# Kernel optimization log

Hardware: AMD Instinct MI355X
Metric: run time of the kernel (lower is better)

## Reference

```python
import jax, jax.numpy as jnp
import numpy as np

B, K, S, L, D, A = 16, 128, 64, 2, 256, 500  # batch, beam, stack, layers, hidden, max_actions


def setup_inputs() -> dict:
    key = jax.random.key(0)
    k = jax.random.split(key, 8)
    return {
        "gen_ll": jax.random.normal(k[0], (B, K), jnp.float32),
        "trees": jax.random.normal(k[1], (B, K, S, D), jnp.float32),
        "hiddens": jax.random.normal(k[2], (B, K, S + 1, L, D), jnp.float32),
        "cells": jax.random.normal(k[3], (B, K, S + 1, L, D), jnp.float32),
        "actions": jax.random.randint(k[4], (B, K, A), 0, 100, dtype=jnp.int64)
        if jax.config.jax_enable_x64 else jax.random.randint(k[4], (B, K, A), 0, 100),
        "actions_pos": jax.random.randint(k[5], (B, K), 0, A - 1),
        "pointer": jax.random.randint(k[6], (B, K), 0, S),
        "beam_widths": jax.random.randint(k[7], (B,), 1, K + 1),  # >= 1 active beam per batch
    }


def _gather_beam(x, sort_idx):
    # gather along beam dim (axis=1) with broadcast over trailing dims
    idx = sort_idx.reshape(sort_idx.shape + (1,) * (x.ndim - 2))
    return jnp.take_along_axis(x, idx, axis=1)


def reference(gen_ll, trees, hiddens, cells, actions, actions_pos, pointer, beam_widths):
    # BeamItems.shrink(): mask beams outside active width, sort by score desc,
    # then reorder every parallel tensor (stack + action path) by sort_idx.
    order = jnp.arange(K)
    active = order[None, :] < beam_widths[:, None]                    # [B, K] active_idx_mask
    gen_ll_m = jnp.where(active, gen_ll, -jnp.inf)
    sort_idx = jnp.argsort(-gen_ll_m, axis=1)                          # descending sort
    gen_ll_s = jnp.take_along_axis(gen_ll_m, sort_idx, axis=1)

    trees_s = _gather_beam(trees, sort_idx)                            # stack.sort_by
    hiddens_s = _gather_beam(hiddens, sort_idx)
    cells_s = _gather_beam(cells, sort_idx)
    actions_s = _gather_beam(actions, sort_idx)                        # action_path.sort_by
    actions_pos_s = jnp.take_along_axis(actions_pos, sort_idx, axis=1)
    pointer_s = jnp.take_along_axis(pointer, sort_idx, axis=1)         # stack_state.sort_by

    new_beam_widths = jnp.minimum(beam_widths, K)
    # BeamItems.marginal_probs(): logsumexp over active beams (inactive already -inf)
    marginal = jax.nn.logsumexp(gen_ll_s, axis=1)                      # [B]
    # ActionPath.prev_actions(): gather at actions_pos
    prev_actions = jnp.take_along_axis(actions_s, actions_pos_s[:, :, None], axis=2)[:, :, 0]

    return (gen_ll_s, trees_s, hiddens_s, cells_s, marginal,
            actions_s, actions_pos_s, pointer_s, prev_actions, new_beam_widths)
```

## Files before the change

### kernel.cpp

```cpp
#include <hip/hip_runtime.h>
#include <math.h>

#define B 16
#define K 128
#define S 64
#define L 2
#define D 256
#define A 500

#define ROW4_TREES 4096
#define ROW4_HID   8320

#define NEG_BIG (-1.0e30f)

#define OFF_GENLL 0
#define OFF_TREES 2048
#define OFF_HID   33556480
#define OFF_CELLS 101713920
#define OFF_MARG  169871360
#define OFF_ACT   169871376
#define OFF_APOS  170895376
#define OFF_PTR   170897424
#define OFF_PREV  170899472
#define OFF_NBW   170901520

#define NB_SORT B
#define NB_ACT  (B * K)
#define NB_BIG  (3 * B * K)
#define GRID (NB_SORT + NB_ACT + NB_BIG)

template<int N4>
__device__ __forceinline__ void copy_row(const float4* __restrict__ s,
                                         float4* __restrict__ d, int tid)
{
    constexpr int FULL = N4 / 256;
    constexpr int REM  = N4 % 256;
#pragma unroll 8
    for (int i = 0; i < FULL; ++i)
        d[i * 256 + tid] = s[i * 256 + tid];
    if (REM && tid < REM)
        d[FULL * 256 + tid] = s[FULL * 256 + tid];
}

__global__ void __launch_bounds__(256)
k_fused(const float* __restrict__ gen_ll,
        const float4* __restrict__ trees,
        const float4* __restrict__ hiddens,
        const float4* __restrict__ cells,
        const int* __restrict__ actions,
        const int* __restrict__ actions_pos,
        const int* __restrict__ pointer,
        const int* __restrict__ beam_widths,
        float* __restrict__ out)
{
    __shared__ float key[K];
    __shared__ int   sidx[K];
    __shared__ float red[4];

    const int tid = threadIdx.x;
    const int bid = blockIdx.x;

    int type, b, k = 0, r = 0, seg = 0;
    if (bid < NB_SORT) {
        type = 0; b = bid;
    } else if (bid < NB_SORT + NB_ACT) {
        type = 1; r = bid - NB_SORT; b = r >> 7; k = r & 127;
    } else {
        type = 2;
        const int idx = bid - (NB_SORT + NB_ACT);
        seg = idx % 3; r = idx / 3; b = r >> 7; k = r & 127;
    }

    const int w = beam_widths[b];
    if (tid < K) key[tid] = (tid < w) ? gen_ll[b * K + tid] : NEG_BIG;
    __syncthreads();
    if (tid < K) {
        const float my = key[tid];
        int rank = 0;
#pragma unroll 16
        for (int i = 0; i < K; ++i) {
            const float ki = key[i];
            rank += (ki > my) || (ki == my && i < tid);
        }
        sidx[rank] = tid;
    }
    __syncthreads();

    if (type == 2) {
        const int j = sidx[k];
        if (seg == 0) {
            copy_row<ROW4_TREES>(trees + (size_t)(b * K + j) * ROW4_TREES,
                                 (float4*)(out + OFF_TREES) + (size_t)r * ROW4_TREES, tid);
        } else {
            const float4* src = (seg == 1) ? hiddens : cells;
            float* dst0 = out + ((seg == 1) ? OFF_HID : OFF_CELLS);
            copy_row<ROW4_HID>(src + (size_t)(b * K + j) * ROW4_HID,
                               (float4*)dst0 + (size_t)r * ROW4_HID, tid);
        }
    } else if (type == 1) {
        const int j = sidx[k];
        const int* s = actions + (size_t)(b * K + j) * A;
        float* d = out + OFF_ACT + (size_t)r * A;
        if (tid < A) d[tid] = (float)s[tid];
        const int t2 = tid + 256;
        if (t2 < A) d[t2] = (float)s[t2];
    } else {
        if (tid < K) {
            const int j = sidx[tid];
            out[OFF_GENLL + b * K + tid] = key[j];
            const int ap = actions_pos[b * K + j];
            out[OFF_APOS + b * K + tid] = (float)ap;
            out[OFF_PTR  + b * K + tid] = (float)pointer[b * K + j];
            out[OFF_PREV + b * K + tid] = (float)actions[(size_t)(b * K + j) * A + ap];
        }
        const float v = (tid < K) ? key[tid] : NEG_BIG;
        if (tid < 128) {
            float m = v;
#pragma unroll
            for (int mask = 32; mask >= 1; mask >>= 1)
                m = fmaxf(m, __shfl_xor(m, mask, 64));
            if ((tid & 63) == 0) red[tid >> 6] = m;
        }
        __syncthreads();
        const float m = fmaxf(red[0], red[1]);
        if (tid < 128) {
            float e = expf(v - m);
#pragma unroll
            for (int mask = 32; mask >= 1; mask >>= 1)
                e += __shfl_xor(e, mask, 64);
            if ((tid & 63) == 0) red[2 + (tid >> 6)] = e;
        }
        __syncthreads();
        if (tid == 0) {
            out[OFF_MARG + b] = m + logf(red[2] + red[3]);
            out[OFF_NBW + b] = (float)(w < K ? w : K);
        }
    }
}

extern "C" void kernel_launch(void* const* d_in, const int* in_sizes, int n_in,
                              void* d_out, int out_size, void* d_ws, size_t ws_size,
                              hipStream_t stream)
{
    const float* gen_ll      = (const float*)d_in[0];
    const float* trees       = (const float*)d_in[1];
    const float* hiddens     = (const float*)d_in[2];
    const float* cells       = (const float*)d_in[3];
    const int*   actions     = (const int*)d_in[4];
    const int*   actions_pos = (const int*)d_in[5];
    const int*   pointer     = (const int*)d_in[6];
    const int*   beam_widths = (const int*)d_in[7];
    float* out = (float*)d_out;

    k_fused<<<GRID, 256, 0, stream>>>(gen_ll, (const float4*)trees,
                                      (const float4*)hiddens, (const float4*)cells,
                                      actions, actions_pos, pointer, beam_widths, out);
}
```

Baseline: 282.6 us.

## Split hidden/cell rows into halves, use nontemporal batched copies, vectorize actions

Hidden and cell rows are split into two half-row work units so the block workload is balanced with the trees rows. The copy loop now issues eight nontemporal vector loads before eight nontemporal stores to raise memory-level parallelism and avoid cache pollution. The action gather is vectorized to int4 loads and float4 stores, blocks are reordered so big copies launch first, and launch bounds request higher occupancy. The trade-off is more blocks, each redoing the per-batch rank sort.

```diff
diff --git a/kernel.cpp b/kernel.cpp
--- a/kernel.cpp
+++ b/kernel.cpp
@@ -10,8 +10,12 @@
 
 #define ROW4_TREES 4096
 #define ROW4_HID   8320
+#define HALF4_HID  4160
 
 #define NEG_BIG (-1.0e30f)
+
+typedef float f32x4 __attribute__((ext_vector_type(4)));
+typedef int   i32x4 __attribute__((ext_vector_type(4)));
 
 #define OFF_GENLL 0
 #define OFF_TREES 2048
@@ -24,29 +28,38 @@
 #define OFF_PREV  170899472
 #define OFF_NBW   170901520
 
-#define NB_SORT B
-#define NB_ACT  (B * K)
-#define NB_BIG  (3 * B * K)
-#define GRID (NB_SORT + NB_ACT + NB_BIG)
+#define NU_TREES 2048
+#define NU_HC    8192
+#define NU_BIG   (NU_TREES + NU_HC)
+#define NB_ACT   (B * K)
+#define GRID     (NU_BIG + NB_ACT + B)
 
 template<int N4>
-__device__ __forceinline__ void copy_row(const float4* __restrict__ s,
-                                         float4* __restrict__ d, int tid)
+__device__ __forceinline__ void copy_unit(const f32x4* __restrict__ s,
+                                          f32x4* __restrict__ d, int tid)
 {
     constexpr int FULL = N4 / 256;
     constexpr int REM  = N4 % 256;
-#pragma unroll 8
-    for (int i = 0; i < FULL; ++i)
-        d[i * 256 + tid] = s[i * 256 + tid];
-    if (REM && tid < REM)
-        d[FULL * 256 + tid] = s[FULL * 256 + tid];
+    for (int g = 0; g < FULL; g += 8) {
+        f32x4 v[8];
+#pragma unroll
+        for (int i = 0; i < 8; ++i)
+            v[i] = __builtin_nontemporal_load(&s[(g + i) * 256 + tid]);
+#pragma unroll
+        for (int i = 0; i < 8; ++i)
+            __builtin_nontemporal_store(v[i], &d[(g + i) * 256 + tid]);
+    }
+    if (REM && tid < REM) {
+        f32x4 v = __builtin_nontemporal_load(&s[FULL * 256 + tid]);
+        __builtin_nontemporal_store(v, &d[FULL * 256 + tid]);
+    }
 }
 
-__global__ void __launch_bounds__(256)
+__global__ void __launch_bounds__(256, 8)
 k_fused(const float* __restrict__ gen_ll,
-        const float4* __restrict__ trees,
-        const float4* __restrict__ hiddens,
-        const float4* __restrict__ cells,
+        const f32x4* __restrict__ trees,
+        const f32x4* __restrict__ hiddens,
+        const f32x4* __restrict__ cells,
         const int* __restrict__ actions,
         const int* __restrict__ actions_pos,
         const int* __restrict__ pointer,
@@ -60,15 +73,24 @@
     const int tid = threadIdx.x;
     const int bid = blockIdx.x;
 
-    int type, b, k = 0, r = 0, seg = 0;
-    if (bid < NB_SORT) {
-        type = 0; b = bid;
-    } else if (bid < NB_SORT + NB_ACT) {
-        type = 1; r = bid - NB_SORT; b = r >> 7; k = r & 127;
+    int type, b = 0, k = 0, r = 0;
+    int which = 0, u2 = 0;
+    if (bid < NU_BIG) {
+        type = 2;
+        if (bid < NU_TREES) {
+            which = -1;
+            r = bid; b = r >> 7; k = r & 127;
+        } else {
+            const int u = bid - NU_TREES;
+            which = u >> 12;
+            u2 = u & 4095;
+            const int row = u2 >> 1;
+            b = row >> 7; k = row & 127;
+        }
+    } else if (bid < NU_BIG + NB_ACT) {
+        type = 1; r = bid - NU_BIG; b = r >> 7; k = r & 127;
     } else {
-        type = 2;
-        const int idx = bid - (NB_SORT + NB_ACT);
-        seg = idx % 3; r = idx / 3; b = r >> 7; k = r & 127;
+        type = 0; b = bid - (NU_BIG + NB_ACT);
     }
 
     const int w = beam_widths[b];
@@ -88,22 +110,28 @@
 
     if (type == 2) {
         const int j = sidx[k];
-        if (seg == 0) {
-            copy_row<ROW4_TREES>(trees + (size_t)(b * K + j) * ROW4_TREES,
-                                 (float4*)(out + OFF_TREES) + (size_t)r * ROW4_TREES, tid);
+        if (which < 0) {
+            copy_unit<ROW4_TREES>(trees + (size_t)(b * K + j) * ROW4_TREES,
+                                  (f32x4*)(out + OFF_TREES) + (size_t)r * ROW4_TREES,
+                                  tid);
         } else {
-            const float4* src = (seg == 1) ? hiddens : cells;
-            float* dst0 = out + ((seg == 1) ? OFF_HID : OFF_CELLS);
-            copy_row<ROW4_HID>(src + (size_t)(b * K + j) * ROW4_HID,
-                               (float4*)dst0 + (size_t)r * ROW4_HID, tid);
+            const int half = u2 & 1;
+            const f32x4* src = (which ? cells : hiddens)
+                             + ((size_t)(b * K + j) * 2 + half) * HALF4_HID;
+            f32x4* dst = (f32x4*)(out + (which ? OFF_CELLS : OFF_HID))
+                       + (size_t)u2 * HALF4_HID;
+            copy_unit<HALF4_HID>(src, dst, tid);
         }
     } else if (type == 1) {
         const int j = sidx[k];
-        const int* s = actions + (size_t)(b * K + j) * A;
-        float* d = out + OFF_ACT + (size_t)r * A;
-        if (tid < A) d[tid] = (float)s[tid];
-        const int t2 = tid + 256;
-        if (t2 < A) d[t2] = (float)s[t2];
+        const i32x4* s = (const i32x4*)actions + (size_t)(b * K + j) * 125;
+        f32x4* d = (f32x4*)(out + OFF_ACT) + (size_t)r * 125;
+        if (tid < 125) {
+            const i32x4 v = __builtin_nontemporal_load(&s[tid]);
+            f32x4 f;
+            f.x = (float)v.x; f.y = (float)v.y; f.z = (float)v.z; f.w = (float)v.w;
+            __builtin_nontemporal_store(f, &d[tid]);
+        }
     } else {
         if (tid < K) {
             const int j = sidx[tid];
@@ -152,7 +180,7 @@
     const int*   beam_widths = (const int*)d_in[7];
     float* out = (float*)d_out;
 
-    k_fused<<<GRID, 256, 0, stream>>>(gen_ll, (const float4*)trees,
-                                      (const float4*)hiddens, (const float4*)cells,
+    k_fused<<<GRID, 256, 0, stream>>>(gen_ll, (const f32x4*)trees,
+                                      (const f32x4*)hiddens, (const f32x4*)cells,
                                       actions, actions_pos, pointer, beam_widths, out);
 }
```

Measured after the change: 259.8 us. 8.1% less time.
